# Kernel optimization log

Hardware: AMD Instinct MI355X
Metric: run time of the kernel (lower is better)

## Reference

```python
import jax, jax.numpy as jnp
import numpy as np

RADIUS = 8.0   # matches init kwarg radius
EPS = 1e-8     # nn.CosineSimilarity eps


def _denorm(p, height, width):
    # kornia denormalize_pixel_coordinates: [-1,1] -> [0, size-1]
    scale = jnp.array([(width - 1) * 0.5, (height - 1) * 0.5], dtype=p.dtype)
    return (p + 1.0) * scale


def setup_inputs() -> dict:
    key = jax.random.key(0)
    k1, k2, k3, k4 = jax.random.split(key, 4)
    B, N, D = 4, 2048, 256
    features = jax.random.normal(k1, (B, N, D), dtype=jnp.float32)
    pts_src = jax.random.uniform(k2, (B, N, 2), dtype=jnp.float32) * 2.0 - 1.0
    pts_dst = jax.random.uniform(k3, (B, B, N, 2), dtype=jnp.float32) * 2.0 - 1.0
    invis_idx = jax.random.randint(k4, (3, 128), 0, N)
    return {"features": features, "pts_src": pts_src, "pts_dst": pts_dst,
            "invis_idx": invis_idx, "height": 480, "width": 640}


def reference(features, pts_src, pts_dst, invis_idx, height, width):
    # features: [B,N,D]; pts_src: [B,N,2]; pts_dst: [B,B,N,2]
    B, N, D = features.shape
    ps = _denorm(jax.lax.stop_gradient(pts_src), height, width)   # [B,N,2]
    pd = _denorm(jax.lax.stop_gradient(pts_dst), height, width)   # [B,B,N,2]

    # squared euclidean distance d2[i,j,n,m] = ||ps[i,n] - pd[i,j,m]||^2
    s_src = jnp.sum(ps * ps, axis=-1)          # [B,N]
    s_dst = jnp.sum(pd * pd, axis=-1)          # [B,B,N]
    cross = jnp.einsum('ind,ijmd->ijnm', ps, pd)
    d2 = s_src[:, None, :, None] + s_dst[:, :, None, :] - 2.0 * cross  # [B,B,N,N]
    mask = d2 <= RADIUS * RADIUS

    # pair p = i*B + j of the flattened [B^2] grid matches src batch j (p % B)
    # with dst batch i (p // B):
    # cos[i,j,n,m] = <features[j,n], features[i,m]> / max(|f_jn|*|f_im|, eps)
    dots = jnp.einsum('jnd,imd->ijnm', features, features)  # [B,B,N,N]
    norms = jnp.sqrt(jnp.sum(features * features, axis=-1))  # [B,N]
    denom = jnp.maximum(norms[None, :, :, None] * norms[:, None, None, :], EPS)
    cos = dots / denom

    cnt = jnp.maximum(jnp.sum(mask), 1).astype(features.dtype)
    return jnp.sum(jnp.where(mask, 1.0 - cos, 0.0)) / cnt
```

## Files before the change

kernel.cpp:

```cpp
#include <hip/hip_runtime.h>

#define BB 4
#define NN 2048
#define DD 256
#define TILE_N 32
#define NPW 8
#define NT (NN / TILE_N)
#define MSPLIT 2
#define MLEN (NN / MSPLIT)
#define MCH (MLEN / 64)
#define WQ_CAP 96
#define NBLK (BB * BB * NT * MSPLIT)

__global__ __launch_bounds__(256) void rnorm_kernel(const float* __restrict__ feat,
                                                    float* __restrict__ rnorm) {
    const int wave = threadIdx.x >> 6;
    const int lane = threadIdx.x & 63;
    const int row  = blockIdx.x * 4 + wave;
    const float4 v = ((const float4*)(feat + (size_t)row * DD))[lane];
    float s = fmaf(v.x, v.x, fmaf(v.y, v.y, fmaf(v.z, v.z, v.w * v.w)));
#pragma unroll
    for (int off = 32; off >= 1; off >>= 1) s += __shfl_xor(s, off, 64);
    if (lane == 0) {
        float rn = rsqrtf(s);
        rn = rn * (1.5f - 0.5f * s * rn * rn);
        rnorm[row] = rn;
    }
}

__global__ __launch_bounds__(256) void scan_kernel(const float* __restrict__ feat,
                                                   const float* __restrict__ pts_src,
                                                   const float* __restrict__ pts_dst,
                                                   const float* __restrict__ rnorm,
                                                   const int* __restrict__ hptr,
                                                   const int* __restrict__ wptr,
                                                   float* __restrict__ psum,
                                                   unsigned int* __restrict__ pcnt) {
    __shared__ float2 spd[MLEN];
    __shared__ unsigned int wq[4][WQ_CAP];
    __shared__ unsigned int wqc[4];
    __shared__ float bsum[4];
    __shared__ unsigned int bcnt[4];
    const int pair  = blockIdx.x >> 7;
    const int tile  = (blockIdx.x >> 1) & (NT - 1);
    const int mhalf = blockIdx.x & 1;
    const int mbase = mhalf * MLEN;
    const int i = pair >> 2;
    const int j = pair & 3;
    const float sx = ((float)(*wptr) - 1.0f) * 0.5f;
    const float sy = ((float)(*hptr) - 1.0f) * 0.5f;

    const int wave = threadIdx.x >> 6;
    const int lane = threadIdx.x & 63;

    {
        const float4* src = (const float4*)(pts_dst) + (size_t)pair * (NN / 2) + mhalf * (MLEN / 2);
        float4* dst = (float4*)spd;
#pragma unroll
        for (int t = 0; t < 2; ++t) {
            const int idx = t * 256 + threadIdx.x;
            float4 v = src[idx];
            v.x = (v.x + 1.0f) * sx;  v.y = (v.y + 1.0f) * sy;
            v.z = (v.z + 1.0f) * sx;  v.w = (v.w + 1.0f) * sy;
            dst[idx] = v;
        }
    }
    if (lane == 0) wqc[wave] = 0u;
    __syncthreads();

    const int nbase = tile * TILE_N + wave * NPW;
    float psx[NPW], psy[NPW];
#pragma unroll
    for (int k = 0; k < NPW; ++k) {
        psx[k] = (pts_src[(size_t)(i * NN + nbase + k) * 2 + 0] + 1.0f) * sx;
        psy[k] = (pts_src[(size_t)(i * NN + nbase + k) * 2 + 1] + 1.0f) * sy;
    }

    for (int c = 0; c < MCH; ++c) {
        const float2 q = spd[c * 64 + lane];
        float d2v[NPW];
#pragma unroll
        for (int k = 0; k < NPW; ++k) {
            const float dx = psx[k] - q.x;
            const float dy = psy[k] - q.y;
            d2v[k] = fmaf(dx, dx, dy * dy);
        }
        const float mn = fminf(fminf(fminf(d2v[0], d2v[1]), fminf(d2v[2], d2v[3])),
                               fminf(fminf(d2v[4], d2v[5]), fminf(d2v[6], d2v[7])));
        if (__ballot(mn <= 64.0f)) {
            const unsigned int m = (unsigned int)(mbase + c * 64 + lane);
#pragma unroll
            for (int k = 0; k < NPW; ++k) {
                if (d2v[k] <= 64.0f) {
                    const unsigned int slot = atomicAdd(&wqc[wave], 1u);
                    if (slot < WQ_CAP) wq[wave][slot] = ((unsigned int)k << 11) | m;
                }
            }
        }
    }

    const unsigned int hc = min(wqc[wave], (unsigned int)WQ_CAP);
    const int g = lane >> 2, sub = lane & 3;
    float lsum = 0.0f;
    for (unsigned int h0 = 0; h0 < hc; h0 += 16) {
        const unsigned int hid = h0 + (unsigned int)g;
        const bool valid = hid < hc;
        float part = 0.0f;
        int n = 0, m = 0;
        if (valid) {
            const unsigned int rec = wq[wave][hid];
            m = (int)(rec & 2047u);
            n = nbase + (int)(rec >> 11);
            const float4* pa = (const float4*)(feat + (size_t)(j * NN + n) * DD);
            const float4* pb = (const float4*)(feat + (size_t)(i * NN + m) * DD);
#pragma unroll
            for (int t = 0; t < 16; ++t) {
                const float4 a = pa[t * 4 + sub];
                const float4 b = pb[t * 4 + sub];
                part = fmaf(a.x, b.x, fmaf(a.y, b.y, fmaf(a.z, b.z, fmaf(a.w, b.w, part))));
            }
        }
        part += __shfl_xor(part, 1, 64);
        part += __shfl_xor(part, 2, 64);
        if (valid && sub == 0)
            lsum += 1.0f - part * rnorm[j * NN + n] * rnorm[i * NN + m];
    }
#pragma unroll
    for (int off = 32; off >= 1; off >>= 1) lsum += __shfl_xor(lsum, off, 64);

    if (lane == 0) { bsum[wave] = lsum; bcnt[wave] = hc; }
    __syncthreads();
    if (threadIdx.x == 0) {
        psum[blockIdx.x] = bsum[0] + bsum[1] + bsum[2] + bsum[3];
        pcnt[blockIdx.x] = bcnt[0] + bcnt[1] + bcnt[2] + bcnt[3];
    }
}

__global__ __launch_bounds__(256) void finalize_kernel(const float* __restrict__ psum,
                                                       const unsigned int* __restrict__ pcnt,
                                                       float* __restrict__ out) {
    float s = 0.0f;
    float c = 0.0f;
    for (int t = threadIdx.x; t < NBLK; t += 256) {
        s += psum[t];
        c += (float)pcnt[t];
    }
#pragma unroll
    for (int off = 32; off >= 1; off >>= 1) {
        s += __shfl_xor(s, off, 64);
        c += __shfl_xor(c, off, 64);
    }
    __shared__ float ss[4], cc[4];
    const int wave = threadIdx.x >> 6;
    const int lane = threadIdx.x & 63;
    if (lane == 0) { ss[wave] = s; cc[wave] = c; }
    __syncthreads();
    if (threadIdx.x == 0) {
        const float S = ss[0] + ss[1] + ss[2] + ss[3];
        const float C = cc[0] + cc[1] + cc[2] + cc[3];
        out[0] = S / fmaxf(C, 1.0f);
    }
}

extern "C" void kernel_launch(void* const* d_in, const int* in_sizes, int n_in,
                              void* d_out, int out_size, void* d_ws, size_t ws_size,
                              hipStream_t stream) {
    const float* feat    = (const float*)d_in[0];
    const float* pts_src = (const float*)d_in[1];
    const float* pts_dst = (const float*)d_in[2];
    const int* hptr = (const int*)d_in[4];
    const int* wptr = (const int*)d_in[5];
    float* out = (float*)d_out;

    float*        psum  = (float*)d_ws;
    unsigned int* pcnt  = (unsigned int*)((char*)d_ws + 8192);
    float*        rnorm = (float*)((char*)d_ws + 16384);

    rnorm_kernel<<<BB * NN / 4, 256, 0, stream>>>(feat, rnorm);
    scan_kernel<<<NBLK, 256, 0, stream>>>(feat, pts_src, pts_dst,
                                          rnorm, hptr, wptr, psum, pcnt);
    finalize_kernel<<<1, 256, 0, stream>>>(psum, pcnt, out);
}
```

Measured before the change: 89.56 us.

## Fuse norm computation into scan kernel and process two dst points per lane

Drops the separate rnorm kernel launch. Each hit now computes the squared norms of both feature rows alongside the dot product and applies a refined rsqrt of their product inline. The candidate scan also reads a float4 per lane so each lane tests two destination points per iteration, halving loop trips and ballots. The cost is two extra FMA accumulators per hit and more registers in exchange for one fewer kernel launch and no workspace round trip.

```diff
diff --git a/kernel.cpp b/kernel.cpp
--- a/kernel.cpp
+++ b/kernel.cpp
@@ -8,35 +8,18 @@
 #define NT (NN / TILE_N)
 #define MSPLIT 2
 #define MLEN (NN / MSPLIT)
-#define MCH (MLEN / 64)
+#define MCH (MLEN / 128)
 #define WQ_CAP 96
 #define NBLK (BB * BB * NT * MSPLIT)
-
-__global__ __launch_bounds__(256) void rnorm_kernel(const float* __restrict__ feat,
-                                                    float* __restrict__ rnorm) {
-    const int wave = threadIdx.x >> 6;
-    const int lane = threadIdx.x & 63;
-    const int row  = blockIdx.x * 4 + wave;
-    const float4 v = ((const float4*)(feat + (size_t)row * DD))[lane];
-    float s = fmaf(v.x, v.x, fmaf(v.y, v.y, fmaf(v.z, v.z, v.w * v.w)));
-#pragma unroll
-    for (int off = 32; off >= 1; off >>= 1) s += __shfl_xor(s, off, 64);
-    if (lane == 0) {
-        float rn = rsqrtf(s);
-        rn = rn * (1.5f - 0.5f * s * rn * rn);
-        rnorm[row] = rn;
-    }
-}
 
 __global__ __launch_bounds__(256) void scan_kernel(const float* __restrict__ feat,
                                                    const float* __restrict__ pts_src,
                                                    const float* __restrict__ pts_dst,
-                                                   const float* __restrict__ rnorm,
                                                    const int* __restrict__ hptr,
                                                    const int* __restrict__ wptr,
                                                    float* __restrict__ psum,
                                                    unsigned int* __restrict__ pcnt) {
-    __shared__ float2 spd[MLEN];
+    __shared__ float4 spd[MLEN / 2];
     __shared__ unsigned int wq[4][WQ_CAP];
     __shared__ unsigned int wqc[4];
     __shared__ float bsum[4];
@@ -55,14 +38,13 @@
 
     {
         const float4* src = (const float4*)(pts_dst) + (size_t)pair * (NN / 2) + mhalf * (MLEN / 2);
-        float4* dst = (float4*)spd;
 #pragma unroll
         for (int t = 0; t < 2; ++t) {
             const int idx = t * 256 + threadIdx.x;
             float4 v = src[idx];
             v.x = (v.x + 1.0f) * sx;  v.y = (v.y + 1.0f) * sy;
             v.z = (v.z + 1.0f) * sx;  v.w = (v.w + 1.0f) * sy;
-            dst[idx] = v;
+            spd[idx] = v;
         }
     }
     if (lane == 0) wqc[wave] = 0u;
@@ -77,23 +59,29 @@
     }
 
     for (int c = 0; c < MCH; ++c) {
-        const float2 q = spd[c * 64 + lane];
-        float d2v[NPW];
+        const float4 q = spd[c * 64 + lane];
+        float d0[NPW], d1[NPW];
 #pragma unroll
         for (int k = 0; k < NPW; ++k) {
-            const float dx = psx[k] - q.x;
-            const float dy = psy[k] - q.y;
-            d2v[k] = fmaf(dx, dx, dy * dy);
+            const float ax = psx[k] - q.x, ay = psy[k] - q.y;
+            const float bx = psx[k] - q.z, by = psy[k] - q.w;
+            d0[k] = fmaf(ax, ax, ay * ay);
+            d1[k] = fmaf(bx, bx, by * by);
         }
-        const float mn = fminf(fminf(fminf(d2v[0], d2v[1]), fminf(d2v[2], d2v[3])),
-                               fminf(fminf(d2v[4], d2v[5]), fminf(d2v[6], d2v[7])));
+        float mn = fminf(d0[0], d1[0]);
+#pragma unroll
+        for (int k = 1; k < NPW; ++k) mn = fminf(mn, fminf(d0[k], d1[k]));
         if (__ballot(mn <= 64.0f)) {
-            const unsigned int m = (unsigned int)(mbase + c * 64 + lane);
+            const unsigned int m2 = (unsigned int)(mbase + c * 128 + 2 * lane);
 #pragma unroll
             for (int k = 0; k < NPW; ++k) {
-                if (d2v[k] <= 64.0f) {
+                if (d0[k] <= 64.0f) {
                     const unsigned int slot = atomicAdd(&wqc[wave], 1u);
-                    if (slot < WQ_CAP) wq[wave][slot] = ((unsigned int)k << 11) | m;
+                    if (slot < WQ_CAP) wq[wave][slot] = ((unsigned int)k << 11) | m2;
+                }
+                if (d1[k] <= 64.0f) {
+                    const unsigned int slot = atomicAdd(&wqc[wave], 1u);
+                    if (slot < WQ_CAP) wq[wave][slot] = ((unsigned int)k << 11) | (m2 + 1u);
                 }
             }
         }
@@ -105,25 +93,30 @@
     for (unsigned int h0 = 0; h0 < hc; h0 += 16) {
         const unsigned int hid = h0 + (unsigned int)g;
         const bool valid = hid < hc;
-        float part = 0.0f;
-        int n = 0, m = 0;
+        float dd = 0.0f, aa = 0.0f, bb = 0.0f;
         if (valid) {
             const unsigned int rec = wq[wave][hid];
-            m = (int)(rec & 2047u);
-            n = nbase + (int)(rec >> 11);
+            const int m = (int)(rec & 2047u);
+            const int n = nbase + (int)(rec >> 11);
             const float4* pa = (const float4*)(feat + (size_t)(j * NN + n) * DD);
             const float4* pb = (const float4*)(feat + (size_t)(i * NN + m) * DD);
 #pragma unroll
             for (int t = 0; t < 16; ++t) {
                 const float4 a = pa[t * 4 + sub];
                 const float4 b = pb[t * 4 + sub];
-                part = fmaf(a.x, b.x, fmaf(a.y, b.y, fmaf(a.z, b.z, fmaf(a.w, b.w, part))));
+                dd = fmaf(a.x, b.x, fmaf(a.y, b.y, fmaf(a.z, b.z, fmaf(a.w, b.w, dd))));
+                aa = fmaf(a.x, a.x, fmaf(a.y, a.y, fmaf(a.z, a.z, fmaf(a.w, a.w, aa))));
+                bb = fmaf(b.x, b.x, fmaf(b.y, b.y, fmaf(b.z, b.z, fmaf(b.w, b.w, bb))));
             }
         }
-        part += __shfl_xor(part, 1, 64);
-        part += __shfl_xor(part, 2, 64);
-        if (valid && sub == 0)
-            lsum += 1.0f - part * rnorm[j * NN + n] * rnorm[i * NN + m];
+        dd += __shfl_xor(dd, 1, 64);  aa += __shfl_xor(aa, 1, 64);  bb += __shfl_xor(bb, 1, 64);
+        dd += __shfl_xor(dd, 2, 64);  aa += __shfl_xor(aa, 2, 64);  bb += __shfl_xor(bb, 2, 64);
+        if (valid && sub == 0) {
+            const float p = aa * bb;
+            float r = rsqrtf(p);
+            r = r * (1.5f - 0.5f * p * r * r);
+            lsum += 1.0f - dd * r;
+        }
     }
 #pragma unroll
     for (int off = 32; off >= 1; off >>= 1) lsum += __shfl_xor(lsum, off, 64);
@@ -174,10 +167,8 @@
 
     float*        psum  = (float*)d_ws;
     unsigned int* pcnt  = (unsigned int*)((char*)d_ws + 8192);
-    float*        rnorm = (float*)((char*)d_ws + 16384);
 
-    rnorm_kernel<<<BB * NN / 4, 256, 0, stream>>>(feat, rnorm);
     scan_kernel<<<NBLK, 256, 0, stream>>>(feat, pts_src, pts_dst,
-                                          rnorm, hptr, wptr, psum, pcnt);
+                                          hptr, wptr, psum, pcnt);
     finalize_kernel<<<1, 256, 0, stream>>>(psum, pcnt, out);
 }
```

Measured after the change: 87.59 us. 1.02x faster.
